# Kernel tuning notes

Hardware: AMD Instinct MI355X
Metric: run time of the kernel (lower is better)

Reference implementation:

```python
import jax, jax.numpy as jnp
import numpy as np

B, C, H, W = 8, 256, 128, 128
N = H * W
TEMP = 0.07
NUM_NEG = 128
HARD_RADIUS = 4
HARD_RATIO = 0.75   # curriculum fully ramped (_current_hard_ratio == hard_ratio_max)
N_HARD = int(NUM_NEG * HARD_RATIO)   # 96
N_RAND = NUM_NEG - N_HARD            # 32
STEP = max(1, H // 16)               # 8
N_POS = ((H + STEP - 1) // STEP) * ((W + STEP - 1) // STEP)  # 256


def setup_inputs() -> dict:
    key = jax.random.key(0)
    ks = jax.random.split(key, 8)
    fmap_rgb = jax.random.normal(ks[0], (B, C, H, W), jnp.float32)
    fmap_depth = jax.random.normal(ks[1], (B, C, H, W), jnp.float32)
    pu = jax.random.uniform(ks[2], (B, H, W), jnp.float32) * (W - 1)
    pv = jax.random.uniform(ks[3], (B, H, W), jnp.float32) * (H - 1)
    projected_coords = jnp.stack([pu, pv], axis=1)  # (B,2,H,W)
    valid_mask = (jax.random.uniform(ks[4], (B, H, W)) < 0.9).astype(jnp.float32)
    rand_idx = jax.random.randint(ks[5], (B, N_RAND), 0, N, dtype=jnp.int32)
    hard_off_u = jax.random.randint(ks[6], (B, N_HARD, N_POS), -HARD_RADIUS, HARD_RADIUS + 1, dtype=jnp.int32)
    hard_off_v = jax.random.randint(ks[7], (B, N_HARD, N_POS), -HARD_RADIUS, HARD_RADIUS + 1, dtype=jnp.int32)
    return {
        'fmap_rgb': fmap_rgb, 'fmap_depth': fmap_depth,
        'projected_coords': projected_coords, 'valid_mask': valid_mask,
        'rand_idx': rand_idx, 'hard_off_u': hard_off_u, 'hard_off_v': hard_off_v,
    }


def _normalize(x):
    # F.normalize(dim=1): x / max(||x||_2, eps)
    n = jnp.sqrt(jnp.sum(x * x, axis=1, keepdims=True))
    return x / jnp.maximum(n, 1e-12)


def _bilinear_sample(f, x, y):
    # grid_sample(mode=bilinear, padding=zeros, align_corners=True); unnormalized
    # coords equal pixel coords (x=proj_u, y=proj_v). f:(B,C,H,W), x,y:(B,H,W) -> (B,C,N)
    Bb, Cc, Hh, Ww = f.shape
    ff = f.reshape(Bb, Cc, Hh * Ww)
    xf = x.reshape(Bb, -1)
    yf = y.reshape(Bb, -1)
    x0 = jnp.floor(xf)
    y0 = jnp.floor(yf)
    wx = xf - x0
    wy = yf - y0
    x0i = x0.astype(jnp.int32)
    y0i = y0.astype(jnp.int32)

    def g(ix, iy):
        valid = (ix >= 0) & (ix < Ww) & (iy >= 0) & (iy < Hh)
        idx = jnp.clip(iy, 0, Hh - 1) * Ww + jnp.clip(ix, 0, Ww - 1)
        v = jnp.take_along_axis(ff, idx[:, None, :], axis=2)
        return v * valid[:, None, :]

    return (((1 - wx) * (1 - wy))[:, None, :] * g(x0i, y0i)
            + (wx * (1 - wy))[:, None, :] * g(x0i + 1, y0i)
            + ((1 - wx) * wy)[:, None, :] * g(x0i, y0i + 1)
            + (wx * wy)[:, None, :] * g(x0i + 1, y0i + 1))


def reference(fmap_rgb, fmap_depth, projected_coords, valid_mask, rand_idx, hard_off_u, hard_off_v):
    rgb = _normalize(fmap_rgb)
    dep = _normalize(fmap_depth)
    proj_u = projected_coords[:, 0]
    proj_v = projected_coords[:, 1]

    rgb_pos = _bilinear_sample(rgb, proj_u, proj_v)        # (B,C,N)
    dep_flat = dep.reshape(B, C, N)
    rgb_flat = rgb.reshape(B, C, N)
    pos_sim = jnp.sum(dep_flat * rgb_pos, axis=1) / TEMP    # (B,N)

    # random negatives via gather + batched matmul
    rgb_rand = jnp.take_along_axis(rgb_flat, rand_idx[:, None, :].astype(jnp.int32), axis=2)  # (B,C,n_rand)
    rand_neg = jnp.einsum('bcn,bck->bkn', dep_flat, rgb_rand) / TEMP  # (B,n_rand,N)

    # hard negatives on coarse grid (step = H//16)
    gh = jnp.arange(0, H, STEP)
    gw = jnp.arange(0, W, STEP)
    ghf, gwf = [a.reshape(-1) for a in jnp.meshgrid(gh, gw, indexing='ij')]
    grid_idx = ghf * W + gwf                                # (n_pos,)
    pos_u = jnp.clip(proj_u[:, ghf, gwf], 0, W - 1).astype(jnp.int32)  # (B,n_pos)
    pos_v = jnp.clip(proj_v[:, ghf, gwf], 0, H - 1).astype(jnp.int32)
    off_u = jnp.where((hard_off_u == 0) & (hard_off_v == 0), 1, hard_off_u)
    hu = jnp.clip(pos_u[:, None, :] + off_u, 0, W - 1)      # (B,n_hard,n_pos)
    hv = jnp.clip(pos_v[:, None, :] + hard_off_v, 0, H - 1)
    hard_idx = (hv * W + hu).reshape(B, -1)                 # (B, n_hard*n_pos)
    rgb_hard = jnp.take_along_axis(rgb_flat, hard_idx[:, None, :], axis=2).reshape(B, C, N_HARD, N_POS)
    dep_grid = dep_flat[:, :, grid_idx]                     # (B,C,n_pos)
    hard_sim = jnp.einsum('bcp,bchp->bhp', dep_grid, rgb_hard) / TEMP  # (B,n_hard,n_pos)

    # logsumexp over [pos; random negs; hard negs] -- hard negs only exist at grid
    # positions (the torch code scatters into a dense -inf (B,n_hard,N) tensor;
    # logaddexp at grid positions is mathematically identical and avoids it).
    lse_base = jax.scipy.special.logsumexp(
        jnp.concatenate([pos_sim[:, None, :], rand_neg], axis=1), axis=1)  # (B,N)
    lse_hard = jax.scipy.special.logsumexp(hard_sim, axis=1)               # (B,n_pos)
    lse = lse_base.at[:, grid_idx].set(jnp.logaddexp(lse_base[:, grid_idx], lse_hard))

    mask = valid_mask.reshape(B, N)
    denom = jnp.maximum(jnp.sum(mask), 1.0)
    loss = jnp.sum((lse - pos_sim) * mask) / denom

    # accuracy (no_grad in torch); max over all negatives, hard ones only at grid idx
    max_neg = jnp.max(rand_neg, axis=1)
    max_neg = max_neg.at[:, grid_idx].max(jnp.max(hard_sim, axis=1))
    correct = ((pos_sim > max_neg) & (mask > 0.5)).astype(jnp.float32)
    accuracy = jnp.sum(correct) / denom * 100.0
    return loss, jax.lax.stop_gradient(accuracy)
```

## Files before the change

### kernel.cpp

```cpp
#include <hip/hip_runtime.h>
#include <cfloat>
#include <math.h>

#define B_ 8
#define C_ 256
#define C2_ (C_/2)
#define H_ 128
#define W_ 128
#define N_ (H_*W_)
#define NRAND 32
#define NHARD 96
#define NPOS 256
#define INV_TEMP (1.0f/0.07f)

typedef __attribute__((ext_vector_type(8))) short short8;
typedef __attribute__((ext_vector_type(4))) float f32x4;

__device__ __forceinline__ unsigned bf16rne(float x) {
    unsigned u = __float_as_uint(x);
    return (u + 0x7FFFu + ((u >> 16) & 1u)) >> 16;
}
__device__ __forceinline__ float blo(unsigned w) { return __uint_as_float(w << 16); }
__device__ __forceinline__ float bhi(unsigned w) { return __uint_as_float(w & 0xFFFF0000u); }

__global__ __launch_bounds__(256, 4) void kA_norm(
        const float* __restrict__ rgb, const float* __restrict__ dep,
        unsigned* __restrict__ rgbT, unsigned* __restrict__ depT) {
    __shared__ __align__(16) uint4 bounce[64 * 32];
    __shared__ float red[4][64];
    __shared__ float invn[64];
    int bi = blockIdx.x;
    int srcsel = bi >> 11;
    int sub = bi & 2047;
    int b  = sub >> 8;
    int p0 = (sub & 255) << 6;
    int t  = threadIdx.x;
    int lane = t & 63, w = t >> 6;

    const float* src = (srcsel ? dep : rgb) + (size_t)b * C_ * N_ + p0 + lane;
    unsigned* dstT = srcsel ? depT : rgbT;
    float v[64];
    float ssq = 0.f;
    #pragma unroll
    for (int k = 0; k < 64; ++k) {
        v[k] = src[(size_t)(w * 64 + k) * N_];
        ssq += v[k] * v[k];
    }
    red[w][lane] = ssq;
    __syncthreads();
    if (t < 64) {
        float s = red[0][t] + red[1][t] + red[2][t] + red[3][t];
        invn[t] = 1.0f / fmaxf(sqrtf(s), 1e-12f);
    }
    __syncthreads();
    float sc = invn[lane];
    int swz = lane & 7;
    #pragma unroll
    for (int j = 0; j < 8; ++j) {
        uint4 q;
        q.x = bf16rne(v[8 * j + 0] * sc) | (bf16rne(v[8 * j + 1] * sc) << 16);
        q.y = bf16rne(v[8 * j + 2] * sc) | (bf16rne(v[8 * j + 3] * sc) << 16);
        q.z = bf16rne(v[8 * j + 4] * sc) | (bf16rne(v[8 * j + 5] * sc) << 16);
        q.w = bf16rne(v[8 * j + 6] * sc) | (bf16rne(v[8 * j + 7] * sc) << 16);
        bounce[lane * 32 + ((w * 8 + j) ^ swz)] = q;
    }
    __syncthreads();
    uint4* dst = (uint4*)(dstT + (size_t)(b * N_ + p0) * C2_);
    #pragma unroll
    for (int it = 0; it < 8; ++it) {
        int idx = it * 256 + t;
        int px = idx >> 5, j = idx & 31;
        dst[idx] = bounce[px * 32 + (j ^ (px & 7))];
    }
}

__global__ __launch_bounds__(256, 4) void k2_main(
        const unsigned* __restrict__ depT, const unsigned* __restrict__ rgbT,
        const float* __restrict__ coords, const int* __restrict__ rand_idx,
        float* __restrict__ lse_base, float* __restrict__ pos_out,
        float* __restrict__ maxneg_out) {
    __shared__ __align__(16) uint4 rs4[32 * 32];
    int bi = blockIdx.x;
    int b  = bi >> 8;
    int p0 = (bi & 255) << 6;
    int t  = threadIdx.x;
    int lane = t & 63, w = t >> 6;
    int l15 = lane & 15, l4 = lane >> 4;

    #pragma unroll
    for (int it = 0; it < 4; ++it) {
        int flat = it * 256 + t;
        int rn = flat >> 5, c8 = flat & 31;
        int idx = rand_idx[b * NRAND + rn];
        const uint4* src = (const uint4*)(rgbT + (size_t)(b * N_ + idx) * C2_);
        rs4[rn * 32 + (c8 ^ (rn & 7))] = src[c8];
    }

    const short8* arow = (const short8*)(depT + (size_t)(b * N_ + p0 + (w << 4) + l15) * C2_);
    short8 afr[8];
    #pragma unroll
    for (int kc = 0; kc < 8; ++kc) afr[kc] = arow[kc * 4 + l4];

    int px = t >> 2, g = t & 3;
    int n  = p0 + px;
    float xf = coords[(size_t)b * 2 * N_ + n];
    float yf = coords[(size_t)b * 2 * N_ + N_ + n];
    float x0 = floorf(xf), y0 = floorf(yf);
    float wx = xf - x0, wy = yf - y0;
    int ix = (int)x0 + (g & 1);
    int iy = (int)y0 + (g >> 1);
    float wgt = ((g & 1) ? wx : 1.f - wx) * ((g & 2) ? wy : 1.f - wy);
    if (ix < 0 || ix >= W_ || iy < 0 || iy >= H_) wgt = 0.f;
    int ixc = min(max(ix, 0), W_ - 1), iyc = min(max(iy, 0), H_ - 1);
    const uint4* nbr4 = (const uint4*)(rgbT + (size_t)(b * N_ + iyc * W_ + ixc) * C2_);

    __syncthreads();

    f32x4 acc0 = {0.f, 0.f, 0.f, 0.f};
    f32x4 acc1 = {0.f, 0.f, 0.f, 0.f};
    const short8* rnd8 = (const short8*)rs4;
    #pragma unroll
    for (int kc = 0; kc < 8; ++kc) {
        int c8 = kc * 4 + l4;
        short8 b0 = rnd8[l15 * 32 + (c8 ^ (l15 & 7))];
        short8 b1 = rnd8[(16 + l15) * 32 + (c8 ^ (l15 & 7))];
        acc0 = __builtin_amdgcn_mfma_f32_16x16x32_bf16(afr[kc], b0, acc0, 0, 0, 0);
        acc1 = __builtin_amdgcn_mfma_f32_16x16x32_bf16(afr[kc], b1, acc1, 0, 0, 0);
    }

    float accN = 0.f;
    const uint4* drow = (const uint4*)(depT + (size_t)(b * N_ + n) * C2_);
    #pragma unroll 4
    for (int c8 = 0; c8 < 32; ++c8) {
        uint4 dq = drow[c8];
        uint4 rq = nbr4[c8];
        accN += blo(dq.x) * blo(rq.x) + bhi(dq.x) * bhi(rq.x)
              + blo(dq.y) * blo(rq.y) + bhi(dq.y) * bhi(rq.y)
              + blo(dq.z) * blo(rq.z) + bhi(dq.z) * bhi(rq.z)
              + blo(dq.w) * blo(rq.w) + bhi(dq.w) * bhi(rq.w);
    }
    __syncthreads();

    float* simsF = (float*)rs4;
    #pragma unroll
    for (int r = 0; r < 4; ++r) {
        int prow = (w << 4) + (l4 << 2) + r;
        int swn = r << 2;
        simsF[prow * 32 + (l15 ^ swn)]        = acc0[r];
        simsF[prow * 32 + (16 + (l15 ^ swn))] = acc1[r];
    }
    __syncthreads();

    const float scale = INV_TEMP;
    float pp = accN * wgt;
    pp += __shfl_xor(pp, 1, 4);
    pp += __shfl_xor(pp, 2, 4);
    float pos = pp * scale;
    const float4* sf = (const float4*)simsF;
    int fsw = px & 3;
    float4 ra = sf[px * 8 + ((g * 2) ^ fsw)];
    float4 rb = sf[px * 8 + (((g * 2) ^ fsw) ^ 1)];
    float r[8] = {ra.x, ra.y, ra.z, ra.w, rb.x, rb.y, rb.z, rb.w};
    float ml = -FLT_MAX;
    #pragma unroll
    for (int j = 0; j < 8; ++j) { r[j] *= scale; ml = fmaxf(ml, r[j]); }
    ml = fmaxf(ml, __shfl_xor(ml, 1, 4));
    ml = fmaxf(ml, __shfl_xor(ml, 2, 4));
    float mneg = ml;
    float mall = fmaxf(mneg, pos);
    float se = 0.f;
    #pragma unroll
    for (int j = 0; j < 8; ++j) se += expf(r[j] - mall);
    se += __shfl_xor(se, 1, 4);
    se += __shfl_xor(se, 2, 4);
    if (g == 0) {
        float lse = mall + logf(se + expf(pos - mall));
        size_t o = (size_t)b * N_ + n;
        lse_base[o]   = lse;
        pos_out[o]    = pos;
        maxneg_out[o] = mneg;
    }
}

__global__ __launch_bounds__(192) void k3_hard(
        const unsigned* __restrict__ depT, const unsigned* __restrict__ rgbT,
        const float* __restrict__ coords, const int* __restrict__ hoffu,
        const int* __restrict__ hoffv, float* __restrict__ lse_hard,
        float* __restrict__ max_hard) {
    __shared__ __align__(16) float dv[256];
    __shared__ float sm_[3], ss_[3];
    int bp = blockIdx.x;
    int b = bp >> 8, p = bp & 255;
    int gy = (p >> 4) * 8, gx = (p & 15) * 8;
    int nn = gy * W_ + gx;
    int t  = threadIdx.x;
    if (t < 128) {
        unsigned wv = depT[(size_t)(b * N_ + nn) * C2_ + t];
        dv[2 * t]     = blo(wv);
        dv[2 * t + 1] = bhi(wv);
    }
    float pu = coords[(size_t)b * 2 * N_ + nn];
    float pv = coords[(size_t)b * 2 * N_ + N_ + nn];
    int iu = (int)fminf(fmaxf(pu, 0.f), (float)(W_ - 1));
    int iv = (int)fminf(fmaxf(pv, 0.f), (float)(H_ - 1));
    int h = t >> 1, half = t & 1;
    int ou = hoffu[((size_t)b * NHARD + h) * NPOS + p];
    int ov = hoffv[((size_t)b * NHARD + h) * NPOS + p];
    __syncthreads();
    if (ou == 0 && ov == 0) ou = 1;
    int hu = min(max(iu + ou, 0), W_ - 1);
    int hv = min(max(iv + ov, 0), H_ - 1);
    const uint4* hvec = (const uint4*)(rgbT + (size_t)(b * N_ + hv * W_ + hu) * C2_)
                        + half * 16;
    const float4* dvv = (const float4*)dv + half * 32;
    float acc = 0.f;
    #pragma unroll 4
    for (int c8 = 0; c8 < 16; ++c8) {
        uint4 q = hvec[c8];
        float4 d0 = dvv[c8 * 2];
        float4 d1 = dvv[c8 * 2 + 1];
        acc += d0.x * blo(q.x) + d0.y * bhi(q.x)
             + d0.z * blo(q.y) + d0.w * bhi(q.y)
             + d1.x * blo(q.z) + d1.y * bhi(q.z)
             + d1.z * blo(q.w) + d1.w * bhi(q.w);
    }
    float sim = (acc + __shfl_xor(acc, 1, 2)) * INV_TEMP;
    float m = sim;
    #pragma unroll
    for (int o = 32; o > 0; o >>= 1) m = fmaxf(m, __shfl_xor(m, o, 64));
    int wid = t >> 6;
    if ((t & 63) == 0) sm_[wid] = m;
    __syncthreads();
    float mm = fmaxf(fmaxf(sm_[0], sm_[1]), sm_[2]);
    float e = (half == 0) ? expf(sim - mm) : 0.f;
    #pragma unroll
    for (int o = 32; o > 0; o >>= 1) e += __shfl_xor(e, o, 64);
    if ((t & 63) == 0) ss_[wid] = e;
    __syncthreads();
    if (t == 0) {
        lse_hard[bp] = mm + logf(ss_[0] + ss_[1] + ss_[2]);
        max_hard[bp] = mm;
    }
}

__global__ __launch_bounds__(256) void k4_reduce(
        const float* __restrict__ lse_base, const float* __restrict__ pos_sim,
        const float* __restrict__ max_neg, const float* __restrict__ mask,
        const float* __restrict__ lse_hard, const float* __restrict__ max_hard,
        float* __restrict__ acc) {
    int i = blockIdx.x * 256 + threadIdx.x;
    float l  = lse_base[i], ps = pos_sim[i], mn = max_neg[i], mk = mask[i];
    int b = i >> 14;
    int n = i & (N_ - 1);
    int y = n >> 7, x = n & 127;
    if (((y & 7) | (x & 7)) == 0) {
        int p = ((y >> 3) << 4) + (x >> 3);
        float lh = lse_hard[(b << 8) + p];
        float mh = max_hard[(b << 8) + p];
        float m = fmaxf(l, lh);
        l  = m + logf(expf(l - m) + expf(lh - m));
        mn = fmaxf(mn, mh);
    }
    float s0 = (l - ps) * mk;
    float s1 = (ps > mn && mk > 0.5f) ? 1.f : 0.f;
    float s2 = mk;
    #pragma unroll
    for (int o = 32; o > 0; o >>= 1) {
        s0 += __shfl_down(s0, o, 64);
        s1 += __shfl_down(s1, o, 64);
        s2 += __shfl_down(s2, o, 64);
    }
    __shared__ float r0[4], r1[4], r2[4];
    int wid = threadIdx.x >> 6;
    if ((threadIdx.x & 63) == 0) { r0[wid] = s0; r1[wid] = s1; r2[wid] = s2; }
    __syncthreads();
    if (threadIdx.x == 0) {
        atomicAdd(&acc[0], r0[0] + r0[1] + r0[2] + r0[3]);
        atomicAdd(&acc[1], r1[0] + r1[1] + r1[2] + r1[3]);
        atomicAdd(&acc[2], r2[0] + r2[1] + r2[2] + r2[3]);
    }
}

__global__ void k5_final(const float* __restrict__ acc, float* __restrict__ out) {
    if (threadIdx.x == 0) {
        float denom = fmaxf(acc[2], 1.0f);
        out[0] = acc[0] / denom;
        out[1] = acc[1] / denom * 100.0f;
    }
}

extern "C" void kernel_launch(void* const* d_in, const int* in_sizes, int n_in,
                              void* d_out, int out_size, void* d_ws, size_t ws_size,
                              hipStream_t stream) {
    const float* rgb     = (const float*)d_in[0];
    const float* dep     = (const float*)d_in[1];
    const float* coords  = (const float*)d_in[2];
    const float* mask    = (const float*)d_in[3];
    const int*   rand_i  = (const int*)d_in[4];
    const int*   hoffu   = (const int*)d_in[5];
    const int*   hoffv   = (const int*)d_in[6];
    float* out = (float*)d_out;
    char*  ws  = (char*)d_ws;

    const size_t RGBT_B = (size_t)B_ * N_ * C_ * 2;
    const size_t PIX_B  = (size_t)B_ * N_ * 4;
    unsigned* rgbT  = (unsigned*)ws;
    unsigned* depT  = (unsigned*)(ws + RGBT_B);
    float* lse_base = (float*)(ws + 2 * RGBT_B);
    float* pos_sim  = (float*)(ws + 2 * RGBT_B + PIX_B);
    float* max_neg  = (float*)(ws + 2 * RGBT_B + 2 * PIX_B);
    float* lse_hard = (float*)(ws + 2 * RGBT_B + 3 * PIX_B);
    float* max_hard = (float*)(ws + 2 * RGBT_B + 3 * PIX_B + 8192);
    float* acc      = (float*)(ws + 2 * RGBT_B + 3 * PIX_B + 2 * 8192);

    hipMemsetAsync(acc, 0, 16, stream);
    kA_norm<<<2 * B_ * (N_ / 64), 256, 0, stream>>>(rgb, dep, rgbT, depT);
    k2_main<<<B_ * (N_ / 64), 256, 0, stream>>>(depT, rgbT, coords, rand_i,
                                                lse_base, pos_sim, max_neg);
    k3_hard<<<B_ * NPOS, 192, 0, stream>>>(depT, rgbT, coords, hoffu, hoffv,
                                           lse_hard, max_hard);
    k4_reduce<<<(B_ * N_) / 256, 256, 0, stream>>>(lse_base, pos_sim, max_neg,
                                                   mask, lse_hard, max_hard, acc);
    k5_final<<<1, 64, 0, stream>>>(acc, out);
}
```

Measured before the change: 415.5 us.

## Restructure normalize kernel and fuse main, hard-negative and final kernels

Rewrites the normalize/transpose kernel to process 128 pixels per block with float2 loads, staging bf16 values in a large swizzled shared tile before rescaling. Merges the main similarity and hard-negative kernels into one launch with interleaved block roles, and folds the final division into the reduction via a last-block counter. Aims to cut launch overhead and improve load coalescing, at the cost of lower occupancy from 64KB shared memory, idle threads in hard blocks, and an extra bf16 rounding step before normalization.

```diff
diff --git a/kernel.cpp b/kernel.cpp
--- a/kernel.cpp
+++ b/kernel.cpp
@@ -23,223 +23,230 @@
 __device__ __forceinline__ float blo(unsigned w) { return __uint_as_float(w << 16); }
 __device__ __forceinline__ float bhi(unsigned w) { return __uint_as_float(w & 0xFFFF0000u); }
 
-__global__ __launch_bounds__(256, 4) void kA_norm(
+__global__ __launch_bounds__(256, 2) void kA_norm(
         const float* __restrict__ rgb, const float* __restrict__ dep,
         unsigned* __restrict__ rgbT, unsigned* __restrict__ depT) {
-    __shared__ __align__(16) uint4 bounce[64 * 32];
-    __shared__ float red[4][64];
-    __shared__ float invn[64];
+    __shared__ unsigned tileW[256 * 64];
+    __shared__ float red[4][128];
+    __shared__ float invn[128];
     int bi = blockIdx.x;
-    int srcsel = bi >> 11;
-    int sub = bi & 2047;
-    int b  = sub >> 8;
-    int p0 = (sub & 255) << 6;
-    int t  = threadIdx.x;
-    int lane = t & 63, w = t >> 6;
-
-    const float* src = (srcsel ? dep : rgb) + (size_t)b * C_ * N_ + p0 + lane;
-    unsigned* dstT = srcsel ? depT : rgbT;
-    float v[64];
-    float ssq = 0.f;
-    #pragma unroll
+    int sel = bi & 1;
+    int sub = bi >> 1;
+    int b   = sub >> 7;
+    int p0  = (sub & 127) << 7;
+    int t = threadIdx.x, q = t & 63, w = t >> 6;
+
+    const float* src = (sel ? dep : rgb) + (size_t)b * C_ * N_ + p0;
+    float ssx = 0.f, ssy = 0.f;
+    #pragma unroll 8
     for (int k = 0; k < 64; ++k) {
-        v[k] = src[(size_t)(w * 64 + k) * N_];
-        ssq += v[k] * v[k];
-    }
-    red[w][lane] = ssq;
+        int c = w * 64 + k;
+        float2 v = ((const float2*)(src + (size_t)c * N_))[q];
+        ssx += v.x * v.x;
+        ssy += v.y * v.y;
+        tileW[c * 64 + (q ^ (c & 63))] = bf16rne(v.x) | (bf16rne(v.y) << 16);
+    }
+    red[w][2 * q]     = ssx;
+    red[w][2 * q + 1] = ssy;
     __syncthreads();
-    if (t < 64) {
+    if (t < 128) {
         float s = red[0][t] + red[1][t] + red[2][t] + red[3][t];
         invn[t] = 1.0f / fmaxf(sqrtf(s), 1e-12f);
     }
     __syncthreads();
-    float sc = invn[lane];
-    int swz = lane & 7;
+    int px = t >> 1, half = t & 1, pp = t >> 2;
+    float sc = invn[px];
+    unsigned sh = (px & 1) * 16;
+    uint4* dst = (uint4*)((sel ? depT : rgbT) + (size_t)(b * N_ + p0 + px) * C2_)
+                 + half * 16;
     #pragma unroll
-    for (int j = 0; j < 8; ++j) {
-        uint4 q;
-        q.x = bf16rne(v[8 * j + 0] * sc) | (bf16rne(v[8 * j + 1] * sc) << 16);
-        q.y = bf16rne(v[8 * j + 2] * sc) | (bf16rne(v[8 * j + 3] * sc) << 16);
-        q.z = bf16rne(v[8 * j + 4] * sc) | (bf16rne(v[8 * j + 5] * sc) << 16);
-        q.w = bf16rne(v[8 * j + 6] * sc) | (bf16rne(v[8 * j + 7] * sc) << 16);
-        bounce[lane * 32 + ((w * 8 + j) ^ swz)] = q;
-    }
-    __syncthreads();
-    uint4* dst = (uint4*)(dstT + (size_t)(b * N_ + p0) * C2_);
-    #pragma unroll
-    for (int it = 0; it < 8; ++it) {
-        int idx = it * 256 + t;
-        int px = idx >> 5, j = idx & 31;
-        dst[idx] = bounce[px * 32 + (j ^ (px & 7))];
-    }
-}
-
-__global__ __launch_bounds__(256, 4) void k2_main(
+    for (int j4 = 0; j4 < 16; ++j4) {
+        unsigned oo[4];
+        #pragma unroll
+        for (int e = 0; e < 4; ++e) {
+            int c0 = half * 128 + j4 * 8 + e * 2;
+            unsigned w0 = tileW[c0 * 64 + (pp ^ (c0 & 63))];
+            unsigned w1 = tileW[(c0 + 1) * 64 + (pp ^ ((c0 + 1) & 63))];
+            float f0 = __uint_as_float(((w0 >> sh) & 0xFFFFu) << 16) * sc;
+            float f1 = __uint_as_float(((w1 >> sh) & 0xFFFFu) << 16) * sc;
+            oo[e] = bf16rne(f0) | (bf16rne(f1) << 16);
+        }
+        dst[j4] = make_uint4(oo[0], oo[1], oo[2], oo[3]);
+    }
+}
+
+__global__ __launch_bounds__(256, 4) void kB_main(
         const unsigned* __restrict__ depT, const unsigned* __restrict__ rgbT,
         const float* __restrict__ coords, const int* __restrict__ rand_idx,
+        const int* __restrict__ hoffu, const int* __restrict__ hoffv,
         float* __restrict__ lse_base, float* __restrict__ pos_out,
-        float* __restrict__ maxneg_out) {
-    __shared__ __align__(16) uint4 rs4[32 * 32];
-    int bi = blockIdx.x;
-    int b  = bi >> 8;
-    int p0 = (bi & 255) << 6;
-    int t  = threadIdx.x;
-    int lane = t & 63, w = t >> 6;
-    int l15 = lane & 15, l4 = lane >> 4;
-
-    #pragma unroll
-    for (int it = 0; it < 4; ++it) {
-        int flat = it * 256 + t;
-        int rn = flat >> 5, c8 = flat & 31;
-        int idx = rand_idx[b * NRAND + rn];
-        const uint4* src = (const uint4*)(rgbT + (size_t)(b * N_ + idx) * C2_);
-        rs4[rn * 32 + (c8 ^ (rn & 7))] = src[c8];
-    }
-
-    const short8* arow = (const short8*)(depT + (size_t)(b * N_ + p0 + (w << 4) + l15) * C2_);
-    short8 afr[8];
-    #pragma unroll
-    for (int kc = 0; kc < 8; ++kc) afr[kc] = arow[kc * 4 + l4];
-
-    int px = t >> 2, g = t & 3;
-    int n  = p0 + px;
-    float xf = coords[(size_t)b * 2 * N_ + n];
-    float yf = coords[(size_t)b * 2 * N_ + N_ + n];
-    float x0 = floorf(xf), y0 = floorf(yf);
-    float wx = xf - x0, wy = yf - y0;
-    int ix = (int)x0 + (g & 1);
-    int iy = (int)y0 + (g >> 1);
-    float wgt = ((g & 1) ? wx : 1.f - wx) * ((g & 2) ? wy : 1.f - wy);
-    if (ix < 0 || ix >= W_ || iy < 0 || iy >= H_) wgt = 0.f;
-    int ixc = min(max(ix, 0), W_ - 1), iyc = min(max(iy, 0), H_ - 1);
-    const uint4* nbr4 = (const uint4*)(rgbT + (size_t)(b * N_ + iyc * W_ + ixc) * C2_);
-
-    __syncthreads();
-
-    f32x4 acc0 = {0.f, 0.f, 0.f, 0.f};
-    f32x4 acc1 = {0.f, 0.f, 0.f, 0.f};
-    const short8* rnd8 = (const short8*)rs4;
-    #pragma unroll
-    for (int kc = 0; kc < 8; ++kc) {
-        int c8 = kc * 4 + l4;
-        short8 b0 = rnd8[l15 * 32 + (c8 ^ (l15 & 7))];
-        short8 b1 = rnd8[(16 + l15) * 32 + (c8 ^ (l15 & 7))];
-        acc0 = __builtin_amdgcn_mfma_f32_16x16x32_bf16(afr[kc], b0, acc0, 0, 0, 0);
-        acc1 = __builtin_amdgcn_mfma_f32_16x16x32_bf16(afr[kc], b1, acc1, 0, 0, 0);
-    }
-
-    float accN = 0.f;
-    const uint4* drow = (const uint4*)(depT + (size_t)(b * N_ + n) * C2_);
-    #pragma unroll 4
-    for (int c8 = 0; c8 < 32; ++c8) {
-        uint4 dq = drow[c8];
-        uint4 rq = nbr4[c8];
-        accN += blo(dq.x) * blo(rq.x) + bhi(dq.x) * bhi(rq.x)
-              + blo(dq.y) * blo(rq.y) + bhi(dq.y) * bhi(rq.y)
-              + blo(dq.z) * blo(rq.z) + bhi(dq.z) * bhi(rq.z)
-              + blo(dq.w) * blo(rq.w) + bhi(dq.w) * bhi(rq.w);
-    }
-    __syncthreads();
-
-    float* simsF = (float*)rs4;
-    #pragma unroll
-    for (int r = 0; r < 4; ++r) {
-        int prow = (w << 4) + (l4 << 2) + r;
-        int swn = r << 2;
-        simsF[prow * 32 + (l15 ^ swn)]        = acc0[r];
-        simsF[prow * 32 + (16 + (l15 ^ swn))] = acc1[r];
-    }
-    __syncthreads();
-
-    const float scale = INV_TEMP;
-    float pp = accN * wgt;
-    pp += __shfl_xor(pp, 1, 4);
-    pp += __shfl_xor(pp, 2, 4);
-    float pos = pp * scale;
-    const float4* sf = (const float4*)simsF;
-    int fsw = px & 3;
-    float4 ra = sf[px * 8 + ((g * 2) ^ fsw)];
-    float4 rb = sf[px * 8 + (((g * 2) ^ fsw) ^ 1)];
-    float r[8] = {ra.x, ra.y, ra.z, ra.w, rb.x, rb.y, rb.z, rb.w};
-    float ml = -FLT_MAX;
-    #pragma unroll
-    for (int j = 0; j < 8; ++j) { r[j] *= scale; ml = fmaxf(ml, r[j]); }
-    ml = fmaxf(ml, __shfl_xor(ml, 1, 4));
-    ml = fmaxf(ml, __shfl_xor(ml, 2, 4));
-    float mneg = ml;
-    float mall = fmaxf(mneg, pos);
-    float se = 0.f;
-    #pragma unroll
-    for (int j = 0; j < 8; ++j) se += expf(r[j] - mall);
-    se += __shfl_xor(se, 1, 4);
-    se += __shfl_xor(se, 2, 4);
-    if (g == 0) {
-        float lse = mall + logf(se + expf(pos - mall));
-        size_t o = (size_t)b * N_ + n;
-        lse_base[o]   = lse;
-        pos_out[o]    = pos;
-        maxneg_out[o] = mneg;
-    }
-}
-
-__global__ __launch_bounds__(192) void k3_hard(
-        const unsigned* __restrict__ depT, const unsigned* __restrict__ rgbT,
-        const float* __restrict__ coords, const int* __restrict__ hoffu,
-        const int* __restrict__ hoffv, float* __restrict__ lse_hard,
+        float* __restrict__ maxneg_out, float* __restrict__ lse_hard,
         float* __restrict__ max_hard) {
-    __shared__ __align__(16) float dv[256];
-    __shared__ float sm_[3], ss_[3];
-    int bp = blockIdx.x;
-    int b = bp >> 8, p = bp & 255;
-    int gy = (p >> 4) * 8, gx = (p & 15) * 8;
-    int nn = gy * W_ + gx;
-    int t  = threadIdx.x;
-    if (t < 128) {
-        unsigned wv = depT[(size_t)(b * N_ + nn) * C2_ + t];
-        dv[2 * t]     = blo(wv);
-        dv[2 * t + 1] = bhi(wv);
-    }
-    float pu = coords[(size_t)b * 2 * N_ + nn];
-    float pv = coords[(size_t)b * 2 * N_ + N_ + nn];
-    int iu = (int)fminf(fmaxf(pu, 0.f), (float)(W_ - 1));
-    int iv = (int)fminf(fmaxf(pv, 0.f), (float)(H_ - 1));
-    int h = t >> 1, half = t & 1;
-    int ou = hoffu[((size_t)b * NHARD + h) * NPOS + p];
-    int ov = hoffv[((size_t)b * NHARD + h) * NPOS + p];
-    __syncthreads();
-    if (ou == 0 && ov == 0) ou = 1;
-    int hu = min(max(iu + ou, 0), W_ - 1);
-    int hv = min(max(iv + ov, 0), H_ - 1);
-    const uint4* hvec = (const uint4*)(rgbT + (size_t)(b * N_ + hv * W_ + hu) * C2_)
-                        + half * 16;
-    const float4* dvv = (const float4*)dv + half * 32;
-    float acc = 0.f;
-    #pragma unroll 4
-    for (int c8 = 0; c8 < 16; ++c8) {
-        uint4 q = hvec[c8];
-        float4 d0 = dvv[c8 * 2];
-        float4 d1 = dvv[c8 * 2 + 1];
-        acc += d0.x * blo(q.x) + d0.y * bhi(q.x)
-             + d0.z * blo(q.y) + d0.w * bhi(q.y)
-             + d1.x * blo(q.z) + d1.y * bhi(q.z)
-             + d1.z * blo(q.w) + d1.w * bhi(q.w);
-    }
-    float sim = (acc + __shfl_xor(acc, 1, 2)) * INV_TEMP;
-    float m = sim;
-    #pragma unroll
-    for (int o = 32; o > 0; o >>= 1) m = fmaxf(m, __shfl_xor(m, o, 64));
-    int wid = t >> 6;
-    if ((t & 63) == 0) sm_[wid] = m;
-    __syncthreads();
-    float mm = fmaxf(fmaxf(sm_[0], sm_[1]), sm_[2]);
-    float e = (half == 0) ? expf(sim - mm) : 0.f;
-    #pragma unroll
-    for (int o = 32; o > 0; o >>= 1) e += __shfl_xor(e, o, 64);
-    if ((t & 63) == 0) ss_[wid] = e;
-    __syncthreads();
-    if (t == 0) {
-        lse_hard[bp] = mm + logf(ss_[0] + ss_[1] + ss_[2]);
-        max_hard[bp] = mm;
+    __shared__ __align__(16) unsigned char smem[16384];
+    int t = threadIdx.x;
+
+    if ((blockIdx.x & 1) == 0) {
+        uint4* rs4 = (uint4*)smem;
+        int bi = blockIdx.x >> 1;
+        int b  = bi >> 8;
+        int p0 = (bi & 255) << 6;
+        int lane = t & 63, w = t >> 6;
+        int l15 = lane & 15, l4 = lane >> 4;
+
+        #pragma unroll
+        for (int it = 0; it < 4; ++it) {
+            int flat = it * 256 + t;
+            int rn = flat >> 5, c8 = flat & 31;
+            int idx = rand_idx[b * NRAND + rn];
+            const uint4* src = (const uint4*)(rgbT + (size_t)(b * N_ + idx) * C2_);
+            rs4[rn * 32 + (c8 ^ (rn & 7))] = src[c8];
+        }
+
+        const short8* arow = (const short8*)(depT + (size_t)(b * N_ + p0 + (w << 4) + l15) * C2_);
+        short8 afr[8];
+        #pragma unroll
+        for (int kc = 0; kc < 8; ++kc) afr[kc] = arow[kc * 4 + l4];
+
+        int px = t >> 2, g = t & 3;
+        int n  = p0 + px;
+        float xf = coords[(size_t)b * 2 * N_ + n];
+        float yf = coords[(size_t)b * 2 * N_ + N_ + n];
+        float x0 = floorf(xf), y0 = floorf(yf);
+        float wx = xf - x0, wy = yf - y0;
+        int ix = (int)x0 + (g & 1);
+        int iy = (int)y0 + (g >> 1);
+        float wgt = ((g & 1) ? wx : 1.f - wx) * ((g & 2) ? wy : 1.f - wy);
+        if (ix < 0 || ix >= W_ || iy < 0 || iy >= H_) wgt = 0.f;
+        int ixc = min(max(ix, 0), W_ - 1), iyc = min(max(iy, 0), H_ - 1);
+        const uint4* nbr4 = (const uint4*)(rgbT + (size_t)(b * N_ + iyc * W_ + ixc) * C2_);
+
+        __syncthreads();
+
+        f32x4 acc0 = {0.f, 0.f, 0.f, 0.f};
+        f32x4 acc1 = {0.f, 0.f, 0.f, 0.f};
+        const short8* rnd8 = (const short8*)rs4;
+        #pragma unroll
+        for (int kc = 0; kc < 8; ++kc) {
+            int c8 = kc * 4 + l4;
+            short8 b0 = rnd8[l15 * 32 + (c8 ^ (l15 & 7))];
+            short8 b1 = rnd8[(16 + l15) * 32 + (c8 ^ (l15 & 7))];
+            acc0 = __builtin_amdgcn_mfma_f32_16x16x32_bf16(afr[kc], b0, acc0, 0, 0, 0);
+            acc1 = __builtin_amdgcn_mfma_f32_16x16x32_bf16(afr[kc], b1, acc1, 0, 0, 0);
+        }
+
+        float accN = 0.f;
+        const uint4* drow = (const uint4*)(depT + (size_t)(b * N_ + n) * C2_);
+        #pragma unroll 4
+        for (int c8 = 0; c8 < 32; ++c8) {
+            uint4 dq = drow[c8];
+            uint4 rq = nbr4[c8];
+            accN += blo(dq.x) * blo(rq.x) + bhi(dq.x) * bhi(rq.x)
+                  + blo(dq.y) * blo(rq.y) + bhi(dq.y) * bhi(rq.y)
+                  + blo(dq.z) * blo(rq.z) + bhi(dq.z) * bhi(rq.z)
+                  + blo(dq.w) * blo(rq.w) + bhi(dq.w) * bhi(rq.w);
+        }
+        __syncthreads();
+
+        float* simsF = (float*)rs4;
+        #pragma unroll
+        for (int r = 0; r < 4; ++r) {
+            int prow = (w << 4) + (l4 << 2) + r;
+            int swn = r << 2;
+            simsF[prow * 32 + (l15 ^ swn)]        = acc0[r];
+            simsF[prow * 32 + (16 + (l15 ^ swn))] = acc1[r];
+        }
+        __syncthreads();
+
+        const float scale = INV_TEMP;
+        float pp = accN * wgt;
+        pp += __shfl_xor(pp, 1, 4);
+        pp += __shfl_xor(pp, 2, 4);
+        float pos = pp * scale;
+        const float4* sf = (const float4*)simsF;
+        int fsw = px & 3;
+        float4 ra = sf[px * 8 + ((g * 2) ^ fsw)];
+        float4 rb = sf[px * 8 + (((g * 2) ^ fsw) ^ 1)];
+        float r[8] = {ra.x, ra.y, ra.z, ra.w, rb.x, rb.y, rb.z, rb.w};
+        float ml = -FLT_MAX;
+        #pragma unroll
+        for (int j = 0; j < 8; ++j) { r[j] *= scale; ml = fmaxf(ml, r[j]); }
+        ml = fmaxf(ml, __shfl_xor(ml, 1, 4));
+        ml = fmaxf(ml, __shfl_xor(ml, 2, 4));
+        float mneg = ml;
+        float mall = fmaxf(mneg, pos);
+        float se = 0.f;
+        #pragma unroll
+        for (int j = 0; j < 8; ++j) se += expf(r[j] - mall);
+        se += __shfl_xor(se, 1, 4);
+        se += __shfl_xor(se, 2, 4);
+        if (g == 0) {
+            float lse = mall + logf(se + expf(pos - mall));
+            size_t o = (size_t)b * N_ + n;
+            lse_base[o]   = lse;
+            pos_out[o]    = pos;
+            maxneg_out[o] = mneg;
+        }
+    } else {
+        float* dv  = (float*)smem;
+        float* sm_ = (float*)(smem + 1024);
+        float* ss_ = (float*)(smem + 1040);
+        int bp = blockIdx.x >> 1;
+        int b = bp >> 8, p = bp & 255;
+        int gy = (p >> 4) * 8, gx = (p & 15) * 8;
+        int nn = gy * W_ + gx;
+        if (t < 128) {
+            unsigned wv = depT[(size_t)(b * N_ + nn) * C2_ + t];
+            dv[2 * t]     = blo(wv);
+            dv[2 * t + 1] = bhi(wv);
+        }
+        float pu = coords[(size_t)b * 2 * N_ + nn];
+        float pv = coords[(size_t)b * 2 * N_ + N_ + nn];
+        int iu = (int)fminf(fmaxf(pu, 0.f), (float)(W_ - 1));
+        int iv = (int)fminf(fmaxf(pv, 0.f), (float)(H_ - 1));
+        int h = t >> 1, half = t & 1;
+        int ou = 1, ov = 0;
+        if (t < 192) {
+            ou = hoffu[((size_t)b * NHARD + h) * NPOS + p];
+            ov = hoffv[((size_t)b * NHARD + h) * NPOS + p];
+        }
+        __syncthreads();
+        float sim = -FLT_MAX;
+        if (t < 192) {
+            if (ou == 0 && ov == 0) ou = 1;
+            int hu = min(max(iu + ou, 0), W_ - 1);
+            int hv = min(max(iv + ov, 0), H_ - 1);
+            const uint4* hvec = (const uint4*)(rgbT + (size_t)(b * N_ + hv * W_ + hu) * C2_)
+                                + half * 16;
+            const float4* dvv = (const float4*)dv + half * 32;
+            float acc = 0.f;
+            #pragma unroll 4
+            for (int c8 = 0; c8 < 16; ++c8) {
+                uint4 q = hvec[c8];
+                float4 d0 = dvv[c8 * 2];
+                float4 d1 = dvv[c8 * 2 + 1];
+                acc += d0.x * blo(q.x) + d0.y * bhi(q.x)
+                     + d0.z * blo(q.y) + d0.w * bhi(q.y)
+                     + d1.x * blo(q.z) + d1.y * bhi(q.z)
+                     + d1.z * blo(q.w) + d1.w * bhi(q.w);
+            }
+            sim = (acc + __shfl_xor(acc, 1, 2)) * INV_TEMP;
+        }
+        float m = sim;
+        #pragma unroll
+        for (int o = 32; o > 0; o >>= 1) m = fmaxf(m, __shfl_xor(m, o, 64));
+        int wid = t >> 6;
+        if ((t & 63) == 0) sm_[wid] = m;
+        __syncthreads();
+        float mm = fmaxf(fmaxf(sm_[0], sm_[1]), fmaxf(sm_[2], sm_[3]));
+        float e = (t < 192 && half == 0) ? expf(sim - mm) : 0.f;
+        #pragma unroll
+        for (int o = 32; o > 0; o >>= 1) e += __shfl_xor(e, o, 64);
+        if ((t & 63) == 0) ss_[wid] = e;
+        __syncthreads();
+        if (t == 0) {
+            lse_hard[bp] = mm + logf(ss_[0] + ss_[1] + ss_[2] + ss_[3]);
+            max_hard[bp] = mm;
+        }
     }
 }
 
@@ -247,7 +254,7 @@
         const float* __restrict__ lse_base, const float* __restrict__ pos_sim,
         const float* __restrict__ max_neg, const float* __restrict__ mask,
         const float* __restrict__ lse_hard, const float* __restrict__ max_hard,
-        float* __restrict__ acc) {
+        float* __restrict__ acc, float* __restrict__ out) {
     int i = blockIdx.x * 256 + threadIdx.x;
     float l  = lse_base[i], ps = pos_sim[i], mn = max_neg[i], mk = mask[i];
     int b = i >> 14;
@@ -278,14 +285,16 @@
         atomicAdd(&acc[0], r0[0] + r0[1] + r0[2] + r0[3]);
         atomicAdd(&acc[1], r1[0] + r1[1] + r1[2] + r1[3]);
         atomicAdd(&acc[2], r2[0] + r2[1] + r2[2] + r2[3]);
-    }
-}
-
-__global__ void k5_final(const float* __restrict__ acc, float* __restrict__ out) {
-    if (threadIdx.x == 0) {
-        float denom = fmaxf(acc[2], 1.0f);
-        out[0] = acc[0] / denom;
-        out[1] = acc[1] / denom * 100.0f;
+        __threadfence();
+        unsigned prev = atomicAdd((unsigned*)&acc[3], 1u);
+        if (prev == gridDim.x - 1) {
+            float t0 = atomicAdd(&acc[0], 0.f);
+            float t1 = atomicAdd(&acc[1], 0.f);
+            float t2 = atomicAdd(&acc[2], 0.f);
+            float denom = fmaxf(t2, 1.0f);
+            out[0] = t0 / denom;
+            out[1] = t1 / denom * 100.0f;
+        }
     }
 }
 
@@ -314,12 +323,12 @@
     float* acc      = (float*)(ws + 2 * RGBT_B + 3 * PIX_B + 2 * 8192);
 
     hipMemsetAsync(acc, 0, 16, stream);
-    kA_norm<<<2 * B_ * (N_ / 64), 256, 0, stream>>>(rgb, dep, rgbT, depT);
-    k2_main<<<B_ * (N_ / 64), 256, 0, stream>>>(depT, rgbT, coords, rand_i,
-                                                lse_base, pos_sim, max_neg);
-    k3_hard<<<B_ * NPOS, 192, 0, stream>>>(depT, rgbT, coords, hoffu, hoffv,
-                                           lse_hard, max_hard);
+    kA_norm<<<2 * B_ * (N_ / 128), 256, 0, stream>>>(rgb, dep, rgbT, depT);
+    kB_main<<<2 * B_ * (N_ / 64), 256, 0, stream>>>(depT, rgbT, coords, rand_i,
+                                                    hoffu, hoffv, lse_base,
+                                                    pos_sim, max_neg,
+                                                    lse_hard, max_hard);
     k4_reduce<<<(B_ * N_) / 256, 256, 0, stream>>>(lse_base, pos_sim, max_neg,
-                                                   mask, lse_hard, max_hard, acc);
-    k5_final<<<1, 64, 0, stream>>>(acc, out);
-}
+                                                   mask, lse_hard, max_hard,
+                                                   acc, out);
+}
```

Result: slower. 478.0 us (+15.1%).
